# Performance work log

Measured on AMD Instinct MI355X. Metric: run time of the kernel, lower is better.

## Reference

```python
import jax, jax.numpy as jnp
import numpy as np

KS = 5
NF = 64
B, H, W = 2, 160, 160


def _conv1x1(x, w, b):
    # x: (B,Ci,H,W), w: (Co,Ci)
    return jnp.einsum('oi,bihw->bohw', w, x) + b[None, :, None, None]


def _conv2x2(x, w, b, dil):
    # x: (B,1,Hp,Wp), w: (64,1,2,2); VALID conv with dilation dil
    y = jax.lax.conv_general_dilated(x, w, (1, 1), 'VALID',
                                     rhs_dilation=(dil, dil),
                                     dimension_numbers=('NCHW', 'OIHW', 'NCHW'))
    return y + b[None, :, None, None]


def _conv_s(x, w, b):
    # conv1 module, mode 's': gather taps (0,0),(1,1),(1,2),(2,1) of each 3x3 patch,
    # then (1,4) conv == linear combo of 4 shifted images.
    h = x.shape[2] - 2
    wd = x.shape[3] - 2
    x0 = x[:, 0]
    taps = jnp.stack([x0[:, 0:h, 0:wd],
                      x0[:, 1:h + 1, 1:wd + 1],
                      x0[:, 1:h + 1, 2:wd + 2],
                      x0[:, 2:h + 2, 1:wd + 1]], axis=1)  # (B,4,h,wd)
    return jnp.einsum('ok,bkhw->bohw', w.reshape(NF, 4), taps) + b[None, :, None, None]


def _construct(c, dense_ps):
    # relu then dense 1x1-conv chain with channel concat, final 1x1 -> 4 channels
    x = jax.nn.relu(c)
    for (wt, bs) in dense_ps[:-1]:
        feat = jax.nn.relu(_conv1x1(x, wt, bs))
        x = jnp.concatenate([x, feat], axis=1)
    wt, bs = dense_ps[-1]
    return _conv1x1(x, wt, bs)


def _ag(x, sigx, sigy, theta, sigr):
    # x: (B,ks,ks,HW); params: (B,HW). Per-pixel anisotropic bilateral kernel.
    ks = x.shape[1]
    r = jnp.arange(ks, dtype=x.dtype) - ks // 2
    sq = (r[:, None] ** 2 + r[None, :] ** 2)[None, :, :, None]  # (1,ks,ks,1)
    sx = sigx[:, None, None, :]
    sy = sigy[:, None, None, :]
    th = theta[:, None, None, :]
    sr = sigr[:, None, None, :]
    spatial = jnp.exp(-sq / (2.0 * sr ** 2))
    disx = jnp.abs(x[:, ks // 2:ks // 2 + 1] - x)       # center row
    disy = jnp.abs(x[:, :, ks // 2:ks // 2 + 1] - x)    # center col
    a = sx * disx
    bb = sy * disy
    color = jnp.exp(-0.5 * (a ** 2 - 2.0 * th * a * bb + bb ** 2))
    kern = spatial * color
    kern = kern / jnp.sum(kern, axis=(1, 2), keepdims=True)
    return jnp.sum(kern * x, axis=(1, 2))  # (B,HW)


def _forward(x_in, conv1x_w, conv1x_b, conv1c_w, conv1c_b, conv1cs_w, conv1cs_b,
             w2, b2, w3, b3, w4, b4, w5, b5, w6, b6):
    dense_ps = [(w2, b2), (w3, b3), (w4, b4), (w5, b5), (w6, b6)]

    def fk(x, mod):
        if mod == 's':
            c = _conv_s(x, conv1cs_w, conv1cs_b)
        elif mod == 'c':
            c = _conv2x2(x, conv1c_w, conv1c_b, 2)
        else:
            c = _conv2x2(x, conv1x_w, conv1x_b, 1)
        return _construct(c, dense_ps)

    def mode_ens(x, p, mod):
        pad = lambda z: jnp.pad(z, ((0, 0), (0, 0), (0, p), (0, p)), mode='reflect')
        r0 = fk(pad(x), mod)
        r2 = jnp.rot90(fk(pad(jnp.rot90(x, 2, (2, 3))), mod), 2, (2, 3))
        r1 = jnp.rot90(fk(pad(jnp.rot90(x, 1, (2, 3))), mod), 3, (2, 3))
        r3 = jnp.rot90(fk(pad(jnp.rot90(x, 3, (2, 3))), mod), 1, (2, 3))
        return (r0 + r2) / 2.0, (r1 + r3) / 2.0

    e1x, e2x = mode_ens(x_in, 1, 'x')
    e1s, e2s = mode_ens(x_in, 2, 's')
    e1c, e2c = mode_ens(x_in, 2, 'c')
    par = (e1x + e2x + e1s + e2s + e1c + e2c) / 6.0  # (B,4,H,W)

    b, c, h, w = x_in.shape
    sigx = jnp.clip(jax.nn.sigmoid(par[:, 0]).reshape(b, -1) + 1e-6, 0.0, 1.0)
    sigy = jnp.clip(jax.nn.sigmoid(par[:, 1]).reshape(b, -1) + 1e-6, 0.0, 1.0)
    theta = jnp.clip(jnp.tanh(par[:, 2]).reshape(b, -1), -1.0, 1.0)
    sigr = jnp.clip(jnp.tanh(par[:, 3]).reshape(b, -1) + 1e-6, -1.0, 1.0)

    ph = KS // 2
    xt = jnp.pad(x_in, ((0, 0), (0, 0), (ph, ph), (ph, ph)))  # zero pad
    # unfold -> (B, KS, KS, H*W)
    patches = jnp.stack([jnp.stack([xt[:, 0, i:i + h, j:j + w].reshape(b, -1)
                                    for j in range(KS)], axis=1)
                         for i in range(KS)], axis=1)
    outs = _ag(patches, sigx * 20.0, sigy * 20.0, theta, sigr * 10.0 + 10.0).reshape(b, c, h, w)
    return outs, sigx, sigy, theta, sigr


def setup_inputs() -> dict:
    key = jax.random.key(0)
    k = jax.random.split(key, 10)
    def kn(kk, shape, fan_in):
        return jax.random.normal(kk, shape, jnp.float32) * np.float32(np.sqrt(2.0 / fan_in))
    zb = lambda n: jnp.zeros((n,), jnp.float32)
    return {
        'x_in': jax.random.normal(k[0], (B, 1, H, W), jnp.float32),
        'conv1x_w': kn(k[1], (NF, 1, 2, 2), 4), 'conv1x_b': zb(NF),
        'conv1c_w': kn(k[2], (NF, 1, 2, 2), 4), 'conv1c_b': zb(NF),
        'conv1cs_w': kn(k[3], (NF, 1, 1, 4), 4), 'conv1cs_b': zb(NF),
        'w2': kn(k[4], (NF, NF), NF), 'b2': zb(NF),
        'w3': kn(k[5], (NF, 2 * NF), 2 * NF), 'b3': zb(NF),
        'w4': kn(k[6], (NF, 3 * NF), 3 * NF), 'b4': zb(NF),
        'w5': kn(k[7], (NF, 4 * NF), 4 * NF), 'b5': zb(NF),
        'w6': kn(k[8], (4, 5 * NF), 5 * NF), 'b6': zb(4),
    }


def reference(x_in, conv1x_w, conv1x_b, conv1c_w, conv1c_b, conv1cs_w, conv1cs_b,
              w2, b2, w3, b3, w4, b4, w5, b5, w6, b6):
    return _forward(x_in, conv1x_w, conv1x_b, conv1c_w, conv1c_b, conv1cs_w, conv1cs_b,
                    w2, b2, w3, b3, w4, b4, w5, b5, w6, b6)
```

## Files before the change

kernel.cpp:

```cpp
#include <hip/hip_runtime.h>
#include <hip/hip_bf16.h>
#include <math.h>
#include <string.h>


#define NN   160
#define NPIX 25600

typedef __attribute__((ext_vector_type(4))) float float4v;
typedef __attribute__((ext_vector_type(8))) unsigned short ushort8;
typedef __attribute__((ext_vector_type(2))) unsigned int uint2v;
typedef __attribute__((ext_vector_type(4))) unsigned int uint4v;
typedef __attribute__((ext_vector_type(8))) __bf16 bf16x8;

#define PINV(x) asm volatile("" : "+v"(x))

__device__ __forceinline__ int refp(int a) { return (a <= NN - 1) ? a : (2 * (NN - 1) - a); }

__device__ __forceinline__ unsigned int pk2(float lo, float hi) {
    float2 f; f.x = lo; f.y = hi;
    __hip_bfloat162 h = __float22bfloat162_rn(f);
    unsigned int u;
    memcpy(&u, &h, 4);
    return u;
}
__device__ __forceinline__ ushort8 cvt8(const float* __restrict__ p) {
    const float4v f0 = *(const float4v*)p;
    const float4v f1 = *(const float4v*)(p + 4);
    uint4v u;
    u[0] = pk2(f0[0], f0[1]); u[1] = pk2(f0[2], f0[3]);
    u[2] = pk2(f1[0], f1[1]); u[3] = pk2(f1[2], f1[3]);
    return __builtin_bit_cast(ushort8, u);
}

template <int NCH>
__device__ __forceinline__ void dense_layer(const ushort8 (&A)[NCH], float4v biasv,
                                            unsigned short* Xs, int w, int lo16, int lq) {
    const int K = NCH * 32;
#pragma unroll
    for (int pp = 0; pp < 2; ++pp) {
        const int px0 = (pp * 2) * 16 + lo16;
        const int px1 = (pp * 2 + 1) * 16 + lo16;
        float4v acc0 = biasv, acc1 = biasv;
#pragma unroll
        for (int s = 0; s < NCH; ++s) {
            const int c8 = s * 4 + lq;
            const bf16x8 bf0 = __builtin_bit_cast(bf16x8, *(const ushort8*)&Xs[c8 * 512 + px0 * 8]);
            const bf16x8 bf1 = __builtin_bit_cast(bf16x8, *(const ushort8*)&Xs[c8 * 512 + px1 * 8]);
            const bf16x8 af  = __builtin_bit_cast(bf16x8, A[s]);
            acc0 = __builtin_amdgcn_mfma_f32_16x16x32_bf16(af, bf0, acc0, 0, 0, 0);
            acc1 = __builtin_amdgcn_mfma_f32_16x16x32_bf16(af, bf1, acc1, 0, 0, 0);
        }
        const int cb = K + w * 16 + lq * 4;
        uint2v o0, o1;
        o0[0] = pk2(fmaxf(acc0[0], 0.0f), fmaxf(acc0[1], 0.0f));
        o0[1] = pk2(fmaxf(acc0[2], 0.0f), fmaxf(acc0[3], 0.0f));
        o1[0] = pk2(fmaxf(acc1[0], 0.0f), fmaxf(acc1[1], 0.0f));
        o1[1] = pk2(fmaxf(acc1[2], 0.0f), fmaxf(acc1[3], 0.0f));
        *(uint2v*)&Xs[(cb >> 3) * 512 + px0 * 8 + (cb & 7)] = o0;
        *(uint2v*)&Xs[(cb >> 3) * 512 + px1 * 8 + (cb & 7)] = o1;
    }
    __syncthreads();
}

__global__
__attribute__((amdgpu_flat_work_group_size(256, 256)))
__attribute__((amdgpu_waves_per_eu(3, 3)))
void bnet_mlp_kernel(
    const float* __restrict__ x,
    const float* __restrict__ wx, const float* __restrict__ bx,
    const float* __restrict__ wcs, const float* __restrict__ bcs,
    const float* __restrict__ wc, const float* __restrict__ bc,
    const float* __restrict__ w2, const float* __restrict__ b2,
    const float* __restrict__ w3, const float* __restrict__ b3,
    const float* __restrict__ w4, const float* __restrict__ b4,
    const float* __restrict__ w5, const float* __restrict__ b5,
    const float* __restrict__ w6,
    float* __restrict__ par)
{
    __shared__ unsigned short Xs[20480];
    float* red = (float*)Xs;

    const int t = threadIdx.x;
    const int lane = t & 63;
    const int lo16 = lane & 15;
    const int lq = lane >> 4;
    const int w = __builtin_amdgcn_readfirstlane(t >> 6);

    const int arow = w * 16 + lo16;
    ushort8 a2[2], a3[4], a4[6], a5[8], a6[3];
#pragma unroll
    for (int s = 0; s < 2; ++s) { a2[s] = cvt8(&w2[arow * 64 + s * 32 + lq * 8]);  PINV(a2[s]); }
#pragma unroll
    for (int s = 0; s < 4; ++s) { a3[s] = cvt8(&w3[arow * 128 + s * 32 + lq * 8]); PINV(a3[s]); }
#pragma unroll
    for (int s = 0; s < 6; ++s) { a4[s] = cvt8(&w4[arow * 192 + s * 32 + lq * 8]); PINV(a4[s]); }
#pragma unroll
    for (int s = 0; s < 8; ++s) { a5[s] = cvt8(&w5[arow * 256 + s * 32 + lq * 8]); PINV(a5[s]); }
#pragma unroll
    for (int c = 0; c < 3; ++c) {
        const int ch = (3 * w + c) * 32;
        if (ch < 320 && lo16 < 4) {
            a6[c] = cvt8(&w6[lo16 * 320 + ch + lq * 8]);
        } else {
            ushort8 z = {0, 0, 0, 0, 0, 0, 0, 0};
            a6[c] = z;
        }
        PINV(a6[c]);
    }
    const float4v b2v = *(const float4v*)&b2[w * 16 + lq * 4];
    const float4v b3v = *(const float4v*)&b3[w * 16 + lq * 4];
    const float4v b4v = *(const float4v*)&b4[w * 16 + lq * 4];
    const float4v b5v = *(const float4v*)&b5[w * 16 + lq * 4];

    const int bid = blockIdx.x;
    const int nit = 12 + (bid < 384 ? 1 : 0);
    const int g0  = (bid < 384) ? bid * 13 : bid * 12 + 384;

    float4v acc6[4];
    int cur_tb = -1;

    for (int it = 0; it < nit; ++it) {
        const int g = g0 + it;
        const int v = g % 12;
        const int tb = g / 12;
        const int tile = tb >> 1;
        const int b = tb & 1;
        const int mode = v >> 2;
        const int k = v & 3;

        __syncthreads();

        if (tb != cur_tb) {
            if (cur_tb >= 0) {
                const int ftile = cur_tb >> 1;
                const int fb = cur_tb & 1;
                if (lq == 0) {
#pragma unroll
                    for (int pt = 0; pt < 4; ++pt)
                        *(float4v*)&red[(((w * 4) + pt) * 16 + lo16) * 4] = acc6[pt];
                }
                __syncthreads();
                if (w == 0) {
                    float4v sv;
#pragma unroll
                    for (int r = 0; r < 4; ++r)
                        sv[r] = red[(((0 * 4) + lq) * 16 + lo16) * 4 + r]
                              + red[(((1 * 4) + lq) * 16 + lo16) * 4 + r]
                              + red[(((2 * 4) + lq) * 16 + lo16) * 4 + r]
                              + red[(((3 * 4) + lq) * 16 + lo16) * 4 + r];
                    const int pixg = ftile * 64 + lq * 16 + lo16;
#pragma unroll
                    for (int r = 0; r < 4; ++r)
                        atomicAdd(&par[(r * 2 + fb) * NPIX + pixg], sv[r]);
                }
                __syncthreads();
            }
#pragma unroll
            for (int pt = 0; pt < 4; ++pt) { float4v z = {0.f, 0.f, 0.f, 0.f}; acc6[pt] = z; }
            cur_tb = tb;
        }

        const float* xb = x + b * NPIX;
        const float* w1 = (mode == 0) ? wx : (mode == 1) ? wcs : wc;
        const float* b1 = (mode == 0) ? bx : (mode == 1) ? bcs : bc;
        int DY[4], DX[4];
        if (mode == 0)      { DY[0]=0; DY[1]=0; DY[2]=1; DY[3]=1;  DX[0]=0; DX[1]=1; DX[2]=0; DX[3]=1; }
        else if (mode == 1) { DY[0]=0; DY[1]=1; DY[2]=1; DY[3]=2;  DX[0]=0; DX[1]=1; DX[2]=2; DX[3]=1; }
        else                { DY[0]=0; DY[1]=0; DY[2]=2; DY[3]=2;  DX[0]=0; DX[1]=2; DX[2]=0; DX[3]=2; }

        const int pix = tile * 64 + lane;
        const int pi = pix / NN;
        const int pj = pix - pi * NN;

        float s4[4];
#pragma unroll
        for (int tt = 0; tt < 4; ++tt) {
            const int dy = DY[tt], dx = DX[tt];
            int r, c;
            if (k == 0)      { r = refp(pi + dy); c = refp(pj + dx); }
            else if (k == 1) { r = refp(pi + dx); c = (pj >= dy) ? (pj - dy) : (dy - pj); }
            else if (k == 2) { r = (pi >= dy) ? (pi - dy) : (dy - pi);
                               c = (pj >= dx) ? (pj - dx) : (dx - pj); }
            else             { r = (pi >= dx) ? (pi - dx) : (dx - pi); c = refp(pj + dy); }
            s4[tt] = xb[r * NN + c];
        }
        float4v b1v[4];
#pragma unroll
        for (int q = 0; q < 4; ++q) b1v[q] = *(const float4v*)&b1[w * 16 + q * 4];
        float co[16];
#pragma unroll
        for (int oo = 0; oo < 16; ++oo) {
            const int o = w * 16 + oo;
            const float4v wv = *(const float4v*)&w1[o * 4];
            float cacc = b1v[oo >> 2][oo & 3];
#pragma unroll
            for (int tt = 0; tt < 4; ++tt) cacc = fmaf(wv[tt], s4[tt], cacc);
            co[oo] = fmaxf(cacc, 0.0f);
        }
        uint4v pka, pkb;
#pragma unroll
        for (int q = 0; q < 4; ++q) {
            pka[q] = pk2(co[2 * q], co[2 * q + 1]);
            pkb[q] = pk2(co[8 + 2 * q], co[9 + 2 * q]);
        }
        *(uint4v*)&Xs[(w * 2) * 512 + lane * 8]     = pka;
        *(uint4v*)&Xs[(w * 2 + 1) * 512 + lane * 8] = pkb;
        __syncthreads();

        dense_layer<2>(a2, b2v, Xs, w, lo16, lq);
        dense_layer<4>(a3, b3v, Xs, w, lo16, lq);
        dense_layer<6>(a4, b4v, Xs, w, lo16, lq);
        dense_layer<8>(a5, b5v, Xs, w, lo16, lq);

#pragma unroll
        for (int pt = 0; pt < 4; ++pt) {
            const int px = pt * 16 + lo16;
#pragma unroll
            for (int c = 0; c < 3; ++c) {
                int chb = (3 * w + c) * 32;
                chb = (chb < 288) ? chb : 288;
                const int c8 = (chb >> 3) + lq;
                const bf16x8 bf = __builtin_bit_cast(
                    bf16x8, *(const ushort8*)&Xs[c8 * 512 + px * 8]);
                const bf16x8 af = __builtin_bit_cast(bf16x8, a6[c]);
                acc6[pt] = __builtin_amdgcn_mfma_f32_16x16x32_bf16(af, bf, acc6[pt], 0, 0, 0);
            }
        }
    }

    __syncthreads();
    {
        const int ftile = cur_tb >> 1;
        const int fb = cur_tb & 1;
        if (lq == 0) {
#pragma unroll
            for (int pt = 0; pt < 4; ++pt)
                *(float4v*)&red[(((w * 4) + pt) * 16 + lo16) * 4] = acc6[pt];
        }
        __syncthreads();
        if (w == 0) {
            float4v sv;
#pragma unroll
            for (int r = 0; r < 4; ++r)
                sv[r] = red[(((0 * 4) + lq) * 16 + lo16) * 4 + r]
                      + red[(((1 * 4) + lq) * 16 + lo16) * 4 + r]
                      + red[(((2 * 4) + lq) * 16 + lo16) * 4 + r]
                      + red[(((3 * 4) + lq) * 16 + lo16) * 4 + r];
            const int pixg = ftile * 64 + lq * 16 + lo16;
#pragma unroll
            for (int r = 0; r < 4; ++r)
                atomicAdd(&par[(r * 2 + fb) * NPIX + pixg], sv[r]);
        }
    }
}

__global__ __launch_bounds__(64) void bnet_bilateral_kernel(
    const float* __restrict__ x, const float* __restrict__ b6,
    float* __restrict__ out)
{
    const int tid = blockIdx.x * 64 + threadIdx.x;
    const int b = tid / NPIX;
    const int pix = tid - b * NPIX;
    const int pi = pix / NN;
    const int pj = pix - pi * NN;

    float* par = out + 2 * NPIX;
    const float inv12 = 1.0f / 12.0f;
    const float p0 = par[(0 + b) * NPIX + pix] * inv12 + b6[0];
    const float p1 = par[(2 + b) * NPIX + pix] * inv12 + b6[1];
    const float p2 = par[(4 + b) * NPIX + pix] * inv12 + b6[2];
    const float p3 = par[(6 + b) * NPIX + pix] * inv12 + b6[3];

    float sigx = 1.0f / (1.0f + __expf(-p0)) + 1e-6f;
    sigx = fminf(fmaxf(sigx, 0.0f), 1.0f);
    float sigy = 1.0f / (1.0f + __expf(-p1)) + 1e-6f;
    sigy = fminf(fmaxf(sigy, 0.0f), 1.0f);
    float t2 = __expf(2.0f * fminf(fmaxf(p2, -15.0f), 15.0f));
    float th = (t2 - 1.0f) / (t2 + 1.0f);
    th = fminf(fmaxf(th, -1.0f), 1.0f);
    float t3 = __expf(2.0f * fminf(fmaxf(p3, -15.0f), 15.0f));
    float sigr = (t3 - 1.0f) / (t3 + 1.0f) + 1e-6f;
    sigr = fminf(fmaxf(sigr, -1.0f), 1.0f);

    par[(0 + b) * NPIX + pix] = sigx;
    par[(2 + b) * NPIX + pix] = sigy;
    par[(4 + b) * NPIX + pix] = th;
    par[(6 + b) * NPIX + pix] = sigr;

    const float sx = sigx * 20.0f;
    const float sy = sigy * 20.0f;
    const float sr = sigr * 10.0f + 10.0f;

    const float* xb = x + b * NPIX;
    float patch[5][5];
#pragma unroll
    for (int ky = 0; ky < 5; ++ky) {
#pragma unroll
        for (int kx = 0; kx < 5; ++kx) {
            const int r = pi + ky - 2, c = pj + kx - 2;
            patch[ky][kx] = (r >= 0 && r < NN && c >= 0 && c < NN) ? xb[r * NN + c] : 0.0f;
        }
    }

    const float inv2sr2 = 1.0f / (2.0f * sr * sr);
    float num = 0.0f, den = 0.0f;
#pragma unroll
    for (int ky = 0; ky < 5; ++ky) {
#pragma unroll
        for (int kx = 0; kx < 5; ++kx) {
            const float v = patch[ky][kx];
            const float dxv = fabsf(patch[2][kx] - v);
            const float dyv = fabsf(patch[ky][2] - v);
            const float a = sx * dxv;
            const float bb = sy * dyv;
            const float sq = (float)((ky - 2) * (ky - 2) + (kx - 2) * (kx - 2));
            const float kern = __expf(-sq * inv2sr2 - 0.5f * (a * a - 2.0f * th * a * bb + bb * bb));
            den += kern;
            num = fmaf(kern, v, num);
        }
    }
    out[tid] = num / den;
}

extern "C" void kernel_launch(void* const* d_in, const int* in_sizes, int n_in,
                              void* d_out, int out_size, void* d_ws, size_t ws_size,
                              hipStream_t stream) {
    const float* x   = (const float*)d_in[0];
    const float* wx  = (const float*)d_in[1];
    const float* bx  = (const float*)d_in[2];
    const float* wc  = (const float*)d_in[3];
    const float* bc  = (const float*)d_in[4];
    const float* wcs = (const float*)d_in[5];
    const float* bcs = (const float*)d_in[6];
    const float* w2  = (const float*)d_in[7];
    const float* b2  = (const float*)d_in[8];
    const float* w3  = (const float*)d_in[9];
    const float* b3  = (const float*)d_in[10];
    const float* w4  = (const float*)d_in[11];
    const float* b4  = (const float*)d_in[12];
    const float* w5  = (const float*)d_in[13];
    const float* b5  = (const float*)d_in[14];
    const float* w6  = (const float*)d_in[15];
    const float* b6  = (const float*)d_in[16];
    float* out = (float*)d_out;

    (void)hipMemsetAsync(out + 2 * NPIX, 0, 8 * NPIX * sizeof(float), stream);

    hipLaunchKernelGGL(bnet_mlp_kernel, dim3(768), dim3(256), 0, stream,
                       x, wx, bx, wcs, bcs, wc, bc,
                       w2, b2, w3, b3, w4, b4, w5, b5, w6,
                       out + 2 * NPIX);

    hipLaunchKernelGGL(bnet_bilateral_kernel, dim3(800), dim3(64), 0, stream,
                       x, b6, out);
}
```

Measured before the change: 168.0 us.

## Remap MFMA work so each wave covers two output tiles over half the pixels

Each wave of the dense-layer MFMA work now owns two 16-channel output blocks over two 16-pixel groups, instead of one output block over all four groups. Each B-fragment loaded from LDS feeds two MFMAs, which halves LDS reads per MFMA. The cost is doubling the weights held in registers, so occupancy drops to 2 waves per EU and the grid shrinks from 768 to 512 blocks, each doing more iterations. The final 320-channel reduction is split into two halves, so the cross-wave reduction only sums two partials.

```diff
diff --git a/kernel.cpp b/kernel.cpp
--- a/kernel.cpp
+++ b/kernel.cpp
@@ -34,38 +34,42 @@
 }
 
 template <int NCH>
-__device__ __forceinline__ void dense_layer(const ushort8 (&A)[NCH], float4v biasv,
-                                            unsigned short* Xs, int w, int lo16, int lq) {
+__device__ __forceinline__ void dense_layer2(const ushort8 (&A)[2][NCH],
+                                             const float* __restrict__ bL,
+                                             unsigned short* Xs,
+                                             int ow, int pw, int lo16, int lq) {
     const int K = NCH * 32;
-#pragma unroll
-    for (int pp = 0; pp < 2; ++pp) {
-        const int px0 = (pp * 2) * 16 + lo16;
-        const int px1 = (pp * 2 + 1) * 16 + lo16;
-        float4v acc0 = biasv, acc1 = biasv;
+    const float4v bv0 = *(const float4v*)&bL[(2 * ow + 0) * 16 + lq * 4];
+    const float4v bv1 = *(const float4v*)&bL[(2 * ow + 1) * 16 + lq * 4];
+#pragma unroll
+    for (int gi = 0; gi < 2; ++gi) {
+        const int px = (2 * pw + gi) * 16 + lo16;
+        float4v acc0 = bv0, acc1 = bv1;
 #pragma unroll
         for (int s = 0; s < NCH; ++s) {
-            const int c8 = s * 4 + lq;
-            const bf16x8 bf0 = __builtin_bit_cast(bf16x8, *(const ushort8*)&Xs[c8 * 512 + px0 * 8]);
-            const bf16x8 bf1 = __builtin_bit_cast(bf16x8, *(const ushort8*)&Xs[c8 * 512 + px1 * 8]);
-            const bf16x8 af  = __builtin_bit_cast(bf16x8, A[s]);
-            acc0 = __builtin_amdgcn_mfma_f32_16x16x32_bf16(af, bf0, acc0, 0, 0, 0);
-            acc1 = __builtin_amdgcn_mfma_f32_16x16x32_bf16(af, bf1, acc1, 0, 0, 0);
-        }
-        const int cb = K + w * 16 + lq * 4;
+            const bf16x8 bf = __builtin_bit_cast(
+                bf16x8, *(const ushort8*)&Xs[(s * 4 + lq) * 512 + px * 8]);
+            acc0 = __builtin_amdgcn_mfma_f32_16x16x32_bf16(
+                __builtin_bit_cast(bf16x8, A[0][s]), bf, acc0, 0, 0, 0);
+            acc1 = __builtin_amdgcn_mfma_f32_16x16x32_bf16(
+                __builtin_bit_cast(bf16x8, A[1][s]), bf, acc1, 0, 0, 0);
+        }
+        const int cb0 = K + (2 * ow) * 16 + lq * 4;
+        const int cb1 = cb0 + 16;
         uint2v o0, o1;
         o0[0] = pk2(fmaxf(acc0[0], 0.0f), fmaxf(acc0[1], 0.0f));
         o0[1] = pk2(fmaxf(acc0[2], 0.0f), fmaxf(acc0[3], 0.0f));
         o1[0] = pk2(fmaxf(acc1[0], 0.0f), fmaxf(acc1[1], 0.0f));
         o1[1] = pk2(fmaxf(acc1[2], 0.0f), fmaxf(acc1[3], 0.0f));
-        *(uint2v*)&Xs[(cb >> 3) * 512 + px0 * 8 + (cb & 7)] = o0;
-        *(uint2v*)&Xs[(cb >> 3) * 512 + px1 * 8 + (cb & 7)] = o1;
+        *(uint2v*)&Xs[(cb0 >> 3) * 512 + px * 8 + (cb0 & 7)] = o0;
+        *(uint2v*)&Xs[(cb1 >> 3) * 512 + px * 8 + (cb1 & 7)] = o1;
     }
     __syncthreads();
 }
 
 __global__
 __attribute__((amdgpu_flat_work_group_size(256, 256)))
-__attribute__((amdgpu_waves_per_eu(3, 3)))
+__attribute__((amdgpu_waves_per_eu(2, 2)))
 void bnet_mlp_kernel(
     const float* __restrict__ x,
     const float* __restrict__ wx, const float* __restrict__ bx,
@@ -86,21 +90,26 @@
     const int lo16 = lane & 15;
     const int lq = lane >> 4;
     const int w = __builtin_amdgcn_readfirstlane(t >> 6);
-
-    const int arow = w * 16 + lo16;
-    ushort8 a2[2], a3[4], a4[6], a5[8], a6[3];
-#pragma unroll
-    for (int s = 0; s < 2; ++s) { a2[s] = cvt8(&w2[arow * 64 + s * 32 + lq * 8]);  PINV(a2[s]); }
-#pragma unroll
-    for (int s = 0; s < 4; ++s) { a3[s] = cvt8(&w3[arow * 128 + s * 32 + lq * 8]); PINV(a3[s]); }
-#pragma unroll
-    for (int s = 0; s < 6; ++s) { a4[s] = cvt8(&w4[arow * 192 + s * 32 + lq * 8]); PINV(a4[s]); }
-#pragma unroll
-    for (int s = 0; s < 8; ++s) { a5[s] = cvt8(&w5[arow * 256 + s * 32 + lq * 8]); PINV(a5[s]); }
-#pragma unroll
-    for (int c = 0; c < 3; ++c) {
-        const int ch = (3 * w + c) * 32;
-        if (ch < 320 && lo16 < 4) {
+    const int ow = w & 1;
+    const int pw = w >> 1;
+
+    ushort8 a2[2][2], a3[2][4], a4[2][6], a5[2][8], a6[5];
+#pragma unroll
+    for (int ot = 0; ot < 2; ++ot) {
+        const int arow = (2 * ow + ot) * 16 + lo16;
+#pragma unroll
+        for (int s = 0; s < 2; ++s) { a2[ot][s] = cvt8(&w2[arow * 64 + s * 32 + lq * 8]);  PINV(a2[ot][s]); }
+#pragma unroll
+        for (int s = 0; s < 4; ++s) { a3[ot][s] = cvt8(&w3[arow * 128 + s * 32 + lq * 8]); PINV(a3[ot][s]); }
+#pragma unroll
+        for (int s = 0; s < 6; ++s) { a4[ot][s] = cvt8(&w4[arow * 192 + s * 32 + lq * 8]); PINV(a4[ot][s]); }
+#pragma unroll
+        for (int s = 0; s < 8; ++s) { a5[ot][s] = cvt8(&w5[arow * 256 + s * 32 + lq * 8]); PINV(a5[ot][s]); }
+    }
+#pragma unroll
+    for (int c = 0; c < 5; ++c) {
+        const int ch = (ow * 5 + c) * 32;
+        if (lo16 < 4) {
             a6[c] = cvt8(&w6[lo16 * 320 + ch + lq * 8]);
         } else {
             ushort8 z = {0, 0, 0, 0, 0, 0, 0, 0};
@@ -108,16 +117,12 @@
         }
         PINV(a6[c]);
     }
-    const float4v b2v = *(const float4v*)&b2[w * 16 + lq * 4];
-    const float4v b3v = *(const float4v*)&b3[w * 16 + lq * 4];
-    const float4v b4v = *(const float4v*)&b4[w * 16 + lq * 4];
-    const float4v b5v = *(const float4v*)&b5[w * 16 + lq * 4];
 
     const int bid = blockIdx.x;
-    const int nit = 12 + (bid < 384 ? 1 : 0);
-    const int g0  = (bid < 384) ? bid * 13 : bid * 12 + 384;
-
-    float4v acc6[4];
+    const int nit = 18 + (bid < 384 ? 1 : 0);
+    const int g0  = (bid < 384) ? bid * 19 : bid * 18 + 384;
+
+    float4v acc6[2];
     int cur_tb = -1;
 
     for (int it = 0; it < nit; ++it) {
@@ -137,19 +142,16 @@
                 const int fb = cur_tb & 1;
                 if (lq == 0) {
 #pragma unroll
-                    for (int pt = 0; pt < 4; ++pt)
-                        *(float4v*)&red[(((w * 4) + pt) * 16 + lo16) * 4] = acc6[pt];
+                    for (int gi = 0; gi < 2; ++gi)
+                        *(float4v*)&red[(ow * 64 + (2 * pw + gi) * 16 + lo16) * 4] = acc6[gi];
                 }
                 __syncthreads();
                 if (w == 0) {
                     float4v sv;
 #pragma unroll
                     for (int r = 0; r < 4; ++r)
-                        sv[r] = red[(((0 * 4) + lq) * 16 + lo16) * 4 + r]
-                              + red[(((1 * 4) + lq) * 16 + lo16) * 4 + r]
-                              + red[(((2 * 4) + lq) * 16 + lo16) * 4 + r]
-                              + red[(((3 * 4) + lq) * 16 + lo16) * 4 + r];
-                    const int pixg = ftile * 64 + lq * 16 + lo16;
+                        sv[r] = red[(lane) * 4 + r] + red[(64 + lane) * 4 + r];
+                    const int pixg = ftile * 64 + lane;
 #pragma unroll
                     for (int r = 0; r < 4; ++r)
                         atomicAdd(&par[(r * 2 + fb) * NPIX + pixg], sv[r]);
@@ -157,7 +159,7 @@
                 __syncthreads();
             }
 #pragma unroll
-            for (int pt = 0; pt < 4; ++pt) { float4v z = {0.f, 0.f, 0.f, 0.f}; acc6[pt] = z; }
+            for (int gi = 0; gi < 2; ++gi) { float4v z = {0.f, 0.f, 0.f, 0.f}; acc6[gi] = z; }
             cur_tb = tb;
         }
 
@@ -208,23 +210,21 @@
         *(uint4v*)&Xs[(w * 2 + 1) * 512 + lane * 8] = pkb;
         __syncthreads();
 
-        dense_layer<2>(a2, b2v, Xs, w, lo16, lq);
-        dense_layer<4>(a3, b3v, Xs, w, lo16, lq);
-        dense_layer<6>(a4, b4v, Xs, w, lo16, lq);
-        dense_layer<8>(a5, b5v, Xs, w, lo16, lq);
-
-#pragma unroll
-        for (int pt = 0; pt < 4; ++pt) {
-            const int px = pt * 16 + lo16;
-#pragma unroll
-            for (int c = 0; c < 3; ++c) {
-                int chb = (3 * w + c) * 32;
-                chb = (chb < 288) ? chb : 288;
-                const int c8 = (chb >> 3) + lq;
+        dense_layer2<2>(a2, b2, Xs, ow, pw, lo16, lq);
+        dense_layer2<4>(a3, b3, Xs, ow, pw, lo16, lq);
+        dense_layer2<6>(a4, b4, Xs, ow, pw, lo16, lq);
+        dense_layer2<8>(a5, b5, Xs, ow, pw, lo16, lq);
+
+#pragma unroll
+        for (int gi = 0; gi < 2; ++gi) {
+            const int px = (2 * pw + gi) * 16 + lo16;
+#pragma unroll
+            for (int c = 0; c < 5; ++c) {
+                const int c8 = (ow * 5 + c) * 4 + lq;
                 const bf16x8 bf = __builtin_bit_cast(
                     bf16x8, *(const ushort8*)&Xs[c8 * 512 + px * 8]);
-                const bf16x8 af = __builtin_bit_cast(bf16x8, a6[c]);
-                acc6[pt] = __builtin_amdgcn_mfma_f32_16x16x32_bf16(af, bf, acc6[pt], 0, 0, 0);
+                acc6[gi] = __builtin_amdgcn_mfma_f32_16x16x32_bf16(
+                    __builtin_bit_cast(bf16x8, a6[c]), bf, acc6[gi], 0, 0, 0);
             }
         }
     }
@@ -235,19 +235,16 @@
         const int fb = cur_tb & 1;
         if (lq == 0) {
 #pragma unroll
-            for (int pt = 0; pt < 4; ++pt)
-                *(float4v*)&red[(((w * 4) + pt) * 16 + lo16) * 4] = acc6[pt];
+            for (int gi = 0; gi < 2; ++gi)
+                *(float4v*)&red[(ow * 64 + (2 * pw + gi) * 16 + lo16) * 4] = acc6[gi];
         }
         __syncthreads();
         if (w == 0) {
             float4v sv;
 #pragma unroll
             for (int r = 0; r < 4; ++r)
-                sv[r] = red[(((0 * 4) + lq) * 16 + lo16) * 4 + r]
-                      + red[(((1 * 4) + lq) * 16 + lo16) * 4 + r]
-                      + red[(((2 * 4) + lq) * 16 + lo16) * 4 + r]
-                      + red[(((3 * 4) + lq) * 16 + lo16) * 4 + r];
-            const int pixg = ftile * 64 + lq * 16 + lo16;
+                sv[r] = red[(lane) * 4 + r] + red[(64 + lane) * 4 + r];
+            const int pixg = ftile * 64 + lane;
 #pragma unroll
             for (int r = 0; r < 4; ++r)
                 atomicAdd(&par[(r * 2 + fb) * NPIX + pixg], sv[r]);
@@ -347,7 +344,7 @@
 
     (void)hipMemsetAsync(out + 2 * NPIX, 0, 8 * NPIX * sizeof(float), stream);
 
-    hipLaunchKernelGGL(bnet_mlp_kernel, dim3(768), dim3(256), 0, stream,
+    hipLaunchKernelGGL(bnet_mlp_kernel, dim3(512), dim3(256), 0, stream,
                        x, wx, bx, wcs, bcs, wc, bc,
                        w2, b2, w3, b3, w4, b4, w5, b5, w6,
                        out + 2 * NPIX);
```

Result: slower. 187.3 us (+11.5%).

## Pre-convert MLP weights to bf16 in a prep kernel and raise occupancy

Applied to the files above, without the earlier changes.

Adds a small prep kernel that converts the fp32 dense-layer weights to a bf16 MFMA-ready layout in a workspace buffer. The main kernel now loads those weights per layer from global/L2 instead of holding all of them in registers for its whole lifetime. This frees VGPRs, so waves_per_eu goes from 3 to 4 and the grid grows from 768 to 1024 blocks with fewer work items per block. The cost is an extra launch and repeated weight loads inside the loop.

```diff
diff --git a/kernel.cpp b/kernel.cpp
--- a/kernel.cpp
+++ b/kernel.cpp
@@ -6,14 +6,19 @@
 
 #define NN   160
 #define NPIX 25600
+
+#define W2OFF 0
+#define W3OFF 512
+#define W4OFF 1536
+#define W5OFF 3072
+#define W6OFF 5120
+#define WSUNITS 5888
 
 typedef __attribute__((ext_vector_type(4))) float float4v;
 typedef __attribute__((ext_vector_type(8))) unsigned short ushort8;
 typedef __attribute__((ext_vector_type(2))) unsigned int uint2v;
 typedef __attribute__((ext_vector_type(4))) unsigned int uint4v;
 typedef __attribute__((ext_vector_type(8))) __bf16 bf16x8;
-
-#define PINV(x) asm volatile("" : "+v"(x))
 
 __device__ __forceinline__ int refp(int a) { return (a <= NN - 1) ? a : (2 * (NN - 1) - a); }
 
@@ -24,19 +29,55 @@
     memcpy(&u, &h, 4);
     return u;
 }
-__device__ __forceinline__ ushort8 cvt8(const float* __restrict__ p) {
-    const float4v f0 = *(const float4v*)p;
-    const float4v f1 = *(const float4v*)(p + 4);
-    uint4v u;
-    u[0] = pk2(f0[0], f0[1]); u[1] = pk2(f0[2], f0[3]);
-    u[2] = pk2(f1[0], f1[1]); u[3] = pk2(f1[2], f1[3]);
-    return __builtin_bit_cast(ushort8, u);
+
+__global__ __launch_bounds__(256) void bnet_prep_kernel(
+    const float* __restrict__ w2, const float* __restrict__ w3,
+    const float* __restrict__ w4, const float* __restrict__ w5,
+    const float* __restrict__ w6, ushort8* __restrict__ ws)
+{
+    const int u = blockIdx.x * 256 + threadIdx.x;
+    const int lq = u & 3;
+    float src[8];
+    if (u < W6OFF) {
+        const float* wp; int K, rel;
+        if (u < W3OFF)      { wp = w2; K = 64;  rel = u; }
+        else if (u < W4OFF) { wp = w3; K = 128; rel = u - W3OFF; }
+        else if (u < W5OFF) { wp = w4; K = 192; rel = u - W4OFF; }
+        else                { wp = w5; K = 256; rel = u - W5OFF; }
+        const int arow = (rel >> 2) & 63;
+        const int s = rel >> 8;
+        const float* p = &wp[arow * K + s * 32 + lq * 8];
+#pragma unroll
+        for (int e = 0; e < 8; ++e) src[e] = p[e];
+    } else {
+        const int rel = u - W6OFF;
+        const int r = (rel >> 2) & 15;
+        const int c = rel >> 6;
+        if (r < 4 && c < 10) {
+            const float* p = &w6[r * 320 + c * 32 + lq * 8];
+#pragma unroll
+            for (int e = 0; e < 8; ++e) src[e] = p[e];
+        } else {
+#pragma unroll
+            for (int e = 0; e < 8; ++e) src[e] = 0.0f;
+        }
+    }
+    uint4v o;
+    o[0] = pk2(src[0], src[1]); o[1] = pk2(src[2], src[3]);
+    o[2] = pk2(src[4], src[5]); o[3] = pk2(src[6], src[7]);
+    ws[u] = __builtin_bit_cast(ushort8, o);
 }
 
 template <int NCH>
-__device__ __forceinline__ void dense_layer(const ushort8 (&A)[NCH], float4v biasv,
+__device__ __forceinline__ void dense_layer(const ushort8* __restrict__ wsL,
+                                            const float* __restrict__ bL,
                                             unsigned short* Xs, int w, int lo16, int lq) {
     const int K = NCH * 32;
+    const int arow = w * 16 + lo16;
+    ushort8 af[NCH];
+#pragma unroll
+    for (int s = 0; s < NCH; ++s) af[s] = wsL[(s * 64 + arow) * 4 + lq];
+    const float4v biasv = *(const float4v*)&bL[w * 16 + lq * 4];
 #pragma unroll
     for (int pp = 0; pp < 2; ++pp) {
         const int px0 = (pp * 2) * 16 + lo16;
@@ -44,12 +85,11 @@
         float4v acc0 = biasv, acc1 = biasv;
 #pragma unroll
         for (int s = 0; s < NCH; ++s) {
-            const int c8 = s * 4 + lq;
-            const bf16x8 bf0 = __builtin_bit_cast(bf16x8, *(const ushort8*)&Xs[c8 * 512 + px0 * 8]);
-            const bf16x8 bf1 = __builtin_bit_cast(bf16x8, *(const ushort8*)&Xs[c8 * 512 + px1 * 8]);
-            const bf16x8 af  = __builtin_bit_cast(bf16x8, A[s]);
-            acc0 = __builtin_amdgcn_mfma_f32_16x16x32_bf16(af, bf0, acc0, 0, 0, 0);
-            acc1 = __builtin_amdgcn_mfma_f32_16x16x32_bf16(af, bf1, acc1, 0, 0, 0);
+            const bf16x8 bf0 = __builtin_bit_cast(bf16x8, *(const ushort8*)&Xs[(s * 4 + lq) * 512 + px0 * 8]);
+            const bf16x8 bf1 = __builtin_bit_cast(bf16x8, *(const ushort8*)&Xs[(s * 4 + lq) * 512 + px1 * 8]);
+            const bf16x8 afv = __builtin_bit_cast(bf16x8, af[s]);
+            acc0 = __builtin_amdgcn_mfma_f32_16x16x32_bf16(afv, bf0, acc0, 0, 0, 0);
+            acc1 = __builtin_amdgcn_mfma_f32_16x16x32_bf16(afv, bf1, acc1, 0, 0, 0);
         }
         const int cb = K + w * 16 + lq * 4;
         uint2v o0, o1;
@@ -65,17 +105,15 @@
 
 __global__
 __attribute__((amdgpu_flat_work_group_size(256, 256)))
-__attribute__((amdgpu_waves_per_eu(3, 3)))
+__attribute__((amdgpu_waves_per_eu(4, 4)))
 void bnet_mlp_kernel(
     const float* __restrict__ x,
     const float* __restrict__ wx, const float* __restrict__ bx,
     const float* __restrict__ wcs, const float* __restrict__ bcs,
     const float* __restrict__ wc, const float* __restrict__ bc,
-    const float* __restrict__ w2, const float* __restrict__ b2,
-    const float* __restrict__ w3, const float* __restrict__ b3,
-    const float* __restrict__ w4, const float* __restrict__ b4,
-    const float* __restrict__ w5, const float* __restrict__ b5,
-    const float* __restrict__ w6,
+    const float* __restrict__ b2, const float* __restrict__ b3,
+    const float* __restrict__ b4, const float* __restrict__ b5,
+    const ushort8* __restrict__ wsb,
     float* __restrict__ par)
 {
     __shared__ unsigned short Xs[20480];
@@ -87,35 +125,9 @@
     const int lq = lane >> 4;
     const int w = __builtin_amdgcn_readfirstlane(t >> 6);
 
-    const int arow = w * 16 + lo16;
-    ushort8 a2[2], a3[4], a4[6], a5[8], a6[3];
-#pragma unroll
-    for (int s = 0; s < 2; ++s) { a2[s] = cvt8(&w2[arow * 64 + s * 32 + lq * 8]);  PINV(a2[s]); }
-#pragma unroll
-    for (int s = 0; s < 4; ++s) { a3[s] = cvt8(&w3[arow * 128 + s * 32 + lq * 8]); PINV(a3[s]); }
-#pragma unroll
-    for (int s = 0; s < 6; ++s) { a4[s] = cvt8(&w4[arow * 192 + s * 32 + lq * 8]); PINV(a4[s]); }
-#pragma unroll
-    for (int s = 0; s < 8; ++s) { a5[s] = cvt8(&w5[arow * 256 + s * 32 + lq * 8]); PINV(a5[s]); }
-#pragma unroll
-    for (int c = 0; c < 3; ++c) {
-        const int ch = (3 * w + c) * 32;
-        if (ch < 320 && lo16 < 4) {
-            a6[c] = cvt8(&w6[lo16 * 320 + ch + lq * 8]);
-        } else {
-            ushort8 z = {0, 0, 0, 0, 0, 0, 0, 0};
-            a6[c] = z;
-        }
-        PINV(a6[c]);
-    }
-    const float4v b2v = *(const float4v*)&b2[w * 16 + lq * 4];
-    const float4v b3v = *(const float4v*)&b3[w * 16 + lq * 4];
-    const float4v b4v = *(const float4v*)&b4[w * 16 + lq * 4];
-    const float4v b5v = *(const float4v*)&b5[w * 16 + lq * 4];
-
     const int bid = blockIdx.x;
-    const int nit = 12 + (bid < 384 ? 1 : 0);
-    const int g0  = (bid < 384) ? bid * 13 : bid * 12 + 384;
+    const int nit = 9 + (bid < 384 ? 1 : 0);
+    const int g0  = (bid < 384) ? bid * 10 : bid * 9 + 384;
 
     float4v acc6[4];
     int cur_tb = -1;
@@ -208,11 +220,15 @@
         *(uint4v*)&Xs[(w * 2 + 1) * 512 + lane * 8] = pkb;
         __syncthreads();
 
-        dense_layer<2>(a2, b2v, Xs, w, lo16, lq);
-        dense_layer<4>(a3, b3v, Xs, w, lo16, lq);
-        dense_layer<6>(a4, b4v, Xs, w, lo16, lq);
-        dense_layer<8>(a5, b5v, Xs, w, lo16, lq);
-
+        dense_layer<2>(wsb + W2OFF, b2, Xs, w, lo16, lq);
+        dense_layer<4>(wsb + W3OFF, b3, Xs, w, lo16, lq);
+        dense_layer<6>(wsb + W4OFF, b4, Xs, w, lo16, lq);
+        dense_layer<8>(wsb + W5OFF, b5, Xs, w, lo16, lq);
+
+        ushort8 a6[3];
+#pragma unroll
+        for (int c = 0; c < 3; ++c)
+            a6[c] = wsb[W6OFF + ((3 * w + c) * 16 + lo16) * 4 + lq];
 #pragma unroll
         for (int pt = 0; pt < 4; ++pt) {
             const int px = pt * 16 + lo16;
@@ -223,8 +239,8 @@
                 const int c8 = (chb >> 3) + lq;
                 const bf16x8 bf = __builtin_bit_cast(
                     bf16x8, *(const ushort8*)&Xs[c8 * 512 + px * 8]);
-                const bf16x8 af = __builtin_bit_cast(bf16x8, a6[c]);
-                acc6[pt] = __builtin_amdgcn_mfma_f32_16x16x32_bf16(af, bf, acc6[pt], 0, 0, 0);
+                acc6[pt] = __builtin_amdgcn_mfma_f32_16x16x32_bf16(
+                    __builtin_bit_cast(bf16x8, a6[c]), bf, acc6[pt], 0, 0, 0);
             }
         }
     }
@@ -344,12 +360,16 @@
     const float* w6  = (const float*)d_in[15];
     const float* b6  = (const float*)d_in[16];
     float* out = (float*)d_out;
+    ushort8* ws = (ushort8*)d_ws;
 
     (void)hipMemsetAsync(out + 2 * NPIX, 0, 8 * NPIX * sizeof(float), stream);
 
-    hipLaunchKernelGGL(bnet_mlp_kernel, dim3(768), dim3(256), 0, stream,
+    hipLaunchKernelGGL(bnet_prep_kernel, dim3(WSUNITS / 256), dim3(256), 0, stream,
+                       w2, w3, w4, w5, w6, ws);
+
+    hipLaunchKernelGGL(bnet_mlp_kernel, dim3(1024), dim3(256), 0, stream,
                        x, wx, bx, wcs, bcs, wc, bc,
-                       w2, b2, w3, b3, w4, b4, w5, b5, w6,
+                       b2, b3, b4, b5, (const ushort8*)ws,
                        out + 2 * NPIX);
 
     hipLaunchKernelGGL(bnet_bilateral_kernel, dim3(800), dim3(64), 0, stream,
```

Result: slower. 184.3 us (+9.7%).

## Process two work items per iteration with dual LDS buffers to halve barriers

Applied to the files above, without the earlier changes.

Each block now handles two (tile,batch,variant) items per loop iteration, using two LDS activation buffers so every dense layer issues four independent MFMA chains and one barrier covers both items. The grid shrinks from 768 to 512 blocks with 18-19 items each, and the occupancy hint drops from three to two waves per EU to leave room for the extra accumulators. Separate accumulators track two tile-batch groups, which means more frequent flushes with atomics. The intent is to reduce synchronisation and latency stalls per item, at the cost of lower occupancy and doubled LDS use.

```diff
diff --git a/kernel.cpp b/kernel.cpp
--- a/kernel.cpp
+++ b/kernel.cpp
@@ -34,38 +34,126 @@
 }
 
 template <int NCH>
-__device__ __forceinline__ void dense_layer(const ushort8 (&A)[NCH], float4v biasv,
-                                            unsigned short* Xs, int w, int lo16, int lq) {
+__device__ __forceinline__ void dense_dual(const ushort8 (&A)[NCH], float4v biasv,
+                                           unsigned short* X0, unsigned short* X1,
+                                           int w, int lo16, int lq) {
     const int K = NCH * 32;
 #pragma unroll
     for (int pp = 0; pp < 2; ++pp) {
         const int px0 = (pp * 2) * 16 + lo16;
         const int px1 = (pp * 2 + 1) * 16 + lo16;
-        float4v acc0 = biasv, acc1 = biasv;
+        float4v aA0 = biasv, aA1 = biasv, aB0 = biasv, aB1 = biasv;
 #pragma unroll
         for (int s = 0; s < NCH; ++s) {
             const int c8 = s * 4 + lq;
-            const bf16x8 bf0 = __builtin_bit_cast(bf16x8, *(const ushort8*)&Xs[c8 * 512 + px0 * 8]);
-            const bf16x8 bf1 = __builtin_bit_cast(bf16x8, *(const ushort8*)&Xs[c8 * 512 + px1 * 8]);
             const bf16x8 af  = __builtin_bit_cast(bf16x8, A[s]);
-            acc0 = __builtin_amdgcn_mfma_f32_16x16x32_bf16(af, bf0, acc0, 0, 0, 0);
-            acc1 = __builtin_amdgcn_mfma_f32_16x16x32_bf16(af, bf1, acc1, 0, 0, 0);
+            const bf16x8 bA0 = __builtin_bit_cast(bf16x8, *(const ushort8*)&X0[c8 * 512 + px0 * 8]);
+            const bf16x8 bB0 = __builtin_bit_cast(bf16x8, *(const ushort8*)&X1[c8 * 512 + px0 * 8]);
+            const bf16x8 bA1 = __builtin_bit_cast(bf16x8, *(const ushort8*)&X0[c8 * 512 + px1 * 8]);
+            const bf16x8 bB1 = __builtin_bit_cast(bf16x8, *(const ushort8*)&X1[c8 * 512 + px1 * 8]);
+            aA0 = __builtin_amdgcn_mfma_f32_16x16x32_bf16(af, bA0, aA0, 0, 0, 0);
+            aB0 = __builtin_amdgcn_mfma_f32_16x16x32_bf16(af, bB0, aB0, 0, 0, 0);
+            aA1 = __builtin_amdgcn_mfma_f32_16x16x32_bf16(af, bA1, aA1, 0, 0, 0);
+            aB1 = __builtin_amdgcn_mfma_f32_16x16x32_bf16(af, bB1, aB1, 0, 0, 0);
         }
         const int cb = K + w * 16 + lq * 4;
-        uint2v o0, o1;
-        o0[0] = pk2(fmaxf(acc0[0], 0.0f), fmaxf(acc0[1], 0.0f));
-        o0[1] = pk2(fmaxf(acc0[2], 0.0f), fmaxf(acc0[3], 0.0f));
-        o1[0] = pk2(fmaxf(acc1[0], 0.0f), fmaxf(acc1[1], 0.0f));
-        o1[1] = pk2(fmaxf(acc1[2], 0.0f), fmaxf(acc1[3], 0.0f));
-        *(uint2v*)&Xs[(cb >> 3) * 512 + px0 * 8 + (cb & 7)] = o0;
-        *(uint2v*)&Xs[(cb >> 3) * 512 + px1 * 8 + (cb & 7)] = o1;
+        uint2v oA0, oA1, oB0, oB1;
+        oA0[0] = pk2(fmaxf(aA0[0], 0.0f), fmaxf(aA0[1], 0.0f));
+        oA0[1] = pk2(fmaxf(aA0[2], 0.0f), fmaxf(aA0[3], 0.0f));
+        oA1[0] = pk2(fmaxf(aA1[0], 0.0f), fmaxf(aA1[1], 0.0f));
+        oA1[1] = pk2(fmaxf(aA1[2], 0.0f), fmaxf(aA1[3], 0.0f));
+        oB0[0] = pk2(fmaxf(aB0[0], 0.0f), fmaxf(aB0[1], 0.0f));
+        oB0[1] = pk2(fmaxf(aB0[2], 0.0f), fmaxf(aB0[3], 0.0f));
+        oB1[0] = pk2(fmaxf(aB1[0], 0.0f), fmaxf(aB1[1], 0.0f));
+        oB1[1] = pk2(fmaxf(aB1[2], 0.0f), fmaxf(aB1[3], 0.0f));
+        *(uint2v*)&X0[(cb >> 3) * 512 + px0 * 8 + (cb & 7)] = oA0;
+        *(uint2v*)&X0[(cb >> 3) * 512 + px1 * 8 + (cb & 7)] = oA1;
+        *(uint2v*)&X1[(cb >> 3) * 512 + px0 * 8 + (cb & 7)] = oB0;
+        *(uint2v*)&X1[(cb >> 3) * 512 + px1 * 8 + (cb & 7)] = oB1;
+    }
+    __syncthreads();
+}
+
+__device__ __forceinline__ void conv_phase(
+    const float* __restrict__ xb, const float* __restrict__ w1,
+    const float* __restrict__ b1, int tile, int mode, int k,
+    unsigned short* X, int w, int lane, int lo16, int lq)
+{
+    int DY[4], DX[4];
+    if (mode == 0)      { DY[0]=0; DY[1]=0; DY[2]=1; DY[3]=1;  DX[0]=0; DX[1]=1; DX[2]=0; DX[3]=1; }
+    else if (mode == 1) { DY[0]=0; DY[1]=1; DY[2]=1; DY[3]=2;  DX[0]=0; DX[1]=1; DX[2]=2; DX[3]=1; }
+    else                { DY[0]=0; DY[1]=0; DY[2]=2; DY[3]=2;  DX[0]=0; DX[1]=2; DX[2]=0; DX[3]=2; }
+
+    const int pix = tile * 64 + lane;
+    const int pi = pix / NN;
+    const int pj = pix - pi * NN;
+
+    float s4[4];
+#pragma unroll
+    for (int tt = 0; tt < 4; ++tt) {
+        const int dy = DY[tt], dx = DX[tt];
+        int r, c;
+        if (k == 0)      { r = refp(pi + dy); c = refp(pj + dx); }
+        else if (k == 1) { r = refp(pi + dx); c = (pj >= dy) ? (pj - dy) : (dy - pj); }
+        else if (k == 2) { r = (pi >= dy) ? (pi - dy) : (dy - pi);
+                           c = (pj >= dx) ? (pj - dx) : (dx - pj); }
+        else             { r = (pi >= dx) ? (pi - dx) : (dx - pi); c = refp(pj + dy); }
+        s4[tt] = xb[r * NN + c];
+    }
+    float4v b1v[4];
+#pragma unroll
+    for (int q = 0; q < 4; ++q) b1v[q] = *(const float4v*)&b1[w * 16 + q * 4];
+    float co[16];
+#pragma unroll
+    for (int oo = 0; oo < 16; ++oo) {
+        const int o = w * 16 + oo;
+        const float4v wv = *(const float4v*)&w1[o * 4];
+        float cacc = b1v[oo >> 2][oo & 3];
+#pragma unroll
+        for (int tt = 0; tt < 4; ++tt) cacc = fmaf(wv[tt], s4[tt], cacc);
+        co[oo] = fmaxf(cacc, 0.0f);
+    }
+    uint4v pka, pkb;
+#pragma unroll
+    for (int q = 0; q < 4; ++q) {
+        pka[q] = pk2(co[2 * q], co[2 * q + 1]);
+        pkb[q] = pk2(co[8 + 2 * q], co[9 + 2 * q]);
+    }
+    *(uint4v*)&X[(w * 2) * 512 + lane * 8]     = pka;
+    *(uint4v*)&X[(w * 2 + 1) * 512 + lane * 8] = pkb;
+}
+
+__device__ __forceinline__ void flush_tb(const float4v (&acc6)[4], int ftb,
+                                         float* red, float* __restrict__ par,
+                                         int w, int lo16, int lq)
+{
+    const int ftile = ftb >> 1;
+    const int fb = ftb & 1;
+    if (lq == 0) {
+#pragma unroll
+        for (int pt = 0; pt < 4; ++pt)
+            *(float4v*)&red[(((w * 4) + pt) * 16 + lo16) * 4] = acc6[pt];
+    }
+    __syncthreads();
+    if (w == 0) {
+        float4v sv;
+#pragma unroll
+        for (int r = 0; r < 4; ++r)
+            sv[r] = red[(((0 * 4) + lq) * 16 + lo16) * 4 + r]
+                  + red[(((1 * 4) + lq) * 16 + lo16) * 4 + r]
+                  + red[(((2 * 4) + lq) * 16 + lo16) * 4 + r]
+                  + red[(((3 * 4) + lq) * 16 + lo16) * 4 + r];
+        const int pixg = ftile * 64 + lq * 16 + lo16;
+#pragma unroll
+        for (int r = 0; r < 4; ++r)
+            atomicAdd(&par[(r * 2 + fb) * NPIX + pixg], sv[r]);
     }
     __syncthreads();
 }
 
 __global__
 __attribute__((amdgpu_flat_work_group_size(256, 256)))
-__attribute__((amdgpu_waves_per_eu(3, 3)))
+__attribute__((amdgpu_waves_per_eu(2, 2)))
 void bnet_mlp_kernel(
     const float* __restrict__ x,
     const float* __restrict__ wx, const float* __restrict__ bx,
@@ -78,8 +166,8 @@
     const float* __restrict__ w6,
     float* __restrict__ par)
 {
-    __shared__ unsigned short Xs[20480];
-    float* red = (float*)Xs;
+    __shared__ unsigned short Xs[2][20480];
+    float* red = (float*)&Xs[0][0];
 
     const int t = threadIdx.x;
     const int lane = t & 63;
@@ -114,104 +202,50 @@
     const float4v b5v = *(const float4v*)&b5[w * 16 + lq * 4];
 
     const int bid = blockIdx.x;
-    const int nit = 12 + (bid < 384 ? 1 : 0);
-    const int g0  = (bid < 384) ? bid * 13 : bid * 12 + 384;
-
-    float4v acc6[4];
-    int cur_tb = -1;
-
-    for (int it = 0; it < nit; ++it) {
-        const int g = g0 + it;
-        const int v = g % 12;
-        const int tb = g / 12;
-        const int tile = tb >> 1;
-        const int b = tb & 1;
-        const int mode = v >> 2;
-        const int k = v & 3;
+    const int nit = 18 + (bid < 384 ? 1 : 0);
+    const int g0  = (bid < 384) ? bid * 19 : bid * 18 + 384;
+
+    float4v acc6A[4], acc6B[4];
+    int cur_tbA = -1, cur_tbB = -1;
+
+    for (int ii = 0; ii < nit; ii += 2) {
+        const bool dual = (ii + 1 < nit);
+        const int gA = g0 + ii;
+        const int gB = dual ? (gA + 1) : gA;
+
+        const int vA = gA % 12, tbA = gA / 12;
+        const int tileA = tbA >> 1, bA = tbA & 1, modeA = vA >> 2, kA = vA & 3;
+        const int vB = gB % 12, tbB = gB / 12;
+        const int tileB = tbB >> 1, bB = tbB & 1, modeB = vB >> 2, kB = vB & 3;
 
         __syncthreads();
 
-        if (tb != cur_tb) {
-            if (cur_tb >= 0) {
-                const int ftile = cur_tb >> 1;
-                const int fb = cur_tb & 1;
-                if (lq == 0) {
-#pragma unroll
-                    for (int pt = 0; pt < 4; ++pt)
-                        *(float4v*)&red[(((w * 4) + pt) * 16 + lo16) * 4] = acc6[pt];
-                }
-                __syncthreads();
-                if (w == 0) {
-                    float4v sv;
-#pragma unroll
-                    for (int r = 0; r < 4; ++r)
-                        sv[r] = red[(((0 * 4) + lq) * 16 + lo16) * 4 + r]
-                              + red[(((1 * 4) + lq) * 16 + lo16) * 4 + r]
-                              + red[(((2 * 4) + lq) * 16 + lo16) * 4 + r]
-                              + red[(((3 * 4) + lq) * 16 + lo16) * 4 + r];
-                    const int pixg = ftile * 64 + lq * 16 + lo16;
-#pragma unroll
-                    for (int r = 0; r < 4; ++r)
-                        atomicAdd(&par[(r * 2 + fb) * NPIX + pixg], sv[r]);
-                }
-                __syncthreads();
-            }
-#pragma unroll
-            for (int pt = 0; pt < 4; ++pt) { float4v z = {0.f, 0.f, 0.f, 0.f}; acc6[pt] = z; }
-            cur_tb = tb;
-        }
-
-        const float* xb = x + b * NPIX;
-        const float* w1 = (mode == 0) ? wx : (mode == 1) ? wcs : wc;
-        const float* b1 = (mode == 0) ? bx : (mode == 1) ? bcs : bc;
-        int DY[4], DX[4];
-        if (mode == 0)      { DY[0]=0; DY[1]=0; DY[2]=1; DY[3]=1;  DX[0]=0; DX[1]=1; DX[2]=0; DX[3]=1; }
-        else if (mode == 1) { DY[0]=0; DY[1]=1; DY[2]=1; DY[3]=2;  DX[0]=0; DX[1]=1; DX[2]=2; DX[3]=1; }
-        else                { DY[0]=0; DY[1]=0; DY[2]=2; DY[3]=2;  DX[0]=0; DX[1]=2; DX[2]=0; DX[3]=2; }
-
-        const int pix = tile * 64 + lane;
-        const int pi = pix / NN;
-        const int pj = pix - pi * NN;
-
-        float s4[4];
-#pragma unroll
-        for (int tt = 0; tt < 4; ++tt) {
-            const int dy = DY[tt], dx = DX[tt];
-            int r, c;
-            if (k == 0)      { r = refp(pi + dy); c = refp(pj + dx); }
-            else if (k == 1) { r = refp(pi + dx); c = (pj >= dy) ? (pj - dy) : (dy - pj); }
-            else if (k == 2) { r = (pi >= dy) ? (pi - dy) : (dy - pi);
-                               c = (pj >= dx) ? (pj - dx) : (dx - pj); }
-            else             { r = (pi >= dx) ? (pi - dx) : (dx - pi); c = refp(pj + dy); }
-            s4[tt] = xb[r * NN + c];
-        }
-        float4v b1v[4];
-#pragma unroll
-        for (int q = 0; q < 4; ++q) b1v[q] = *(const float4v*)&b1[w * 16 + q * 4];
-        float co[16];
-#pragma unroll
-        for (int oo = 0; oo < 16; ++oo) {
-            const int o = w * 16 + oo;
-            const float4v wv = *(const float4v*)&w1[o * 4];
-            float cacc = b1v[oo >> 2][oo & 3];
-#pragma unroll
-            for (int tt = 0; tt < 4; ++tt) cacc = fmaf(wv[tt], s4[tt], cacc);
-            co[oo] = fmaxf(cacc, 0.0f);
-        }
-        uint4v pka, pkb;
-#pragma unroll
-        for (int q = 0; q < 4; ++q) {
-            pka[q] = pk2(co[2 * q], co[2 * q + 1]);
-            pkb[q] = pk2(co[8 + 2 * q], co[9 + 2 * q]);
-        }
-        *(uint4v*)&Xs[(w * 2) * 512 + lane * 8]     = pka;
-        *(uint4v*)&Xs[(w * 2 + 1) * 512 + lane * 8] = pkb;
+        if (tbA != cur_tbA) {
+            if (cur_tbA >= 0) flush_tb(acc6A, cur_tbA, red, par, w, lo16, lq);
+#pragma unroll
+            for (int pt = 0; pt < 4; ++pt) { float4v z = {0.f, 0.f, 0.f, 0.f}; acc6A[pt] = z; }
+            cur_tbA = tbA;
+        }
+        if (dual && tbB != cur_tbB) {
+            if (cur_tbB >= 0) flush_tb(acc6B, cur_tbB, red, par, w, lo16, lq);
+#pragma unroll
+            for (int pt = 0; pt < 4; ++pt) { float4v z = {0.f, 0.f, 0.f, 0.f}; acc6B[pt] = z; }
+            cur_tbB = tbB;
+        }
+
+        const float* w1A = (modeA == 0) ? wx : (modeA == 1) ? wcs : wc;
+        const float* b1A = (modeA == 0) ? bx : (modeA == 1) ? bcs : bc;
+        const float* w1B = (modeB == 0) ? wx : (modeB == 1) ? wcs : wc;
+        const float* b1B = (modeB == 0) ? bx : (modeB == 1) ? bcs : bc;
+
+        conv_phase(x + bA * NPIX, w1A, b1A, tileA, modeA, kA, &Xs[0][0], w, lane, lo16, lq);
+        conv_phase(x + bB * NPIX, w1B, b1B, tileB, modeB, kB, &Xs[1][0], w, lane, lo16, lq);
         __syncthreads();
 
-        dense_layer<2>(a2, b2v, Xs, w, lo16, lq);
-        dense_layer<4>(a3, b3v, Xs, w, lo16, lq);
-        dense_layer<6>(a4, b4v, Xs, w, lo16, lq);
-        dense_layer<8>(a5, b5v, Xs, w, lo16, lq);
+        dense_dual<2>(a2, b2v, &Xs[0][0], &Xs[1][0], w, lo16, lq);
+        dense_dual<4>(a3, b3v, &Xs[0][0], &Xs[1][0], w, lo16, lq);
+        dense_dual<6>(a4, b4v, &Xs[0][0], &Xs[1][0], w, lo16, lq);
+        dense_dual<8>(a5, b5v, &Xs[0][0], &Xs[1][0], w, lo16, lq);
 
 #pragma unroll
         for (int pt = 0; pt < 4; ++pt) {
@@ -222,37 +256,32 @@
                 chb = (chb < 288) ? chb : 288;
                 const int c8 = (chb >> 3) + lq;
                 const bf16x8 bf = __builtin_bit_cast(
-                    bf16x8, *(const ushort8*)&Xs[c8 * 512 + px * 8]);
-                const bf16x8 af = __builtin_bit_cast(bf16x8, a6[c]);
-                acc6[pt] = __builtin_amdgcn_mfma_f32_16x16x32_bf16(af, bf, acc6[pt], 0, 0, 0);
+                    bf16x8, *(const ushort8*)&Xs[0][c8 * 512 + px * 8]);
+                acc6A[pt] = __builtin_amdgcn_mfma_f32_16x16x32_bf16(
+                    __builtin_bit_cast(bf16x8, a6[c]), bf, acc6A[pt], 0, 0, 0);
             }
         }
+        if (dual) {
+#pragma unroll
+            for (int pt = 0; pt < 4; ++pt) {
+                const int px = pt * 16 + lo16;
+#pragma unroll
+                for (int c = 0; c < 3; ++c) {
+                    int chb = (3 * w + c) * 32;
+                    chb = (chb < 288) ? chb : 288;
+                    const int c8 = (chb >> 3) + lq;
+                    const bf16x8 bf = __builtin_bit_cast(
+                        bf16x8, *(const ushort8*)&Xs[1][c8 * 512 + px * 8]);
+                    acc6B[pt] = __builtin_amdgcn_mfma_f32_16x16x32_bf16(
+                        __builtin_bit_cast(bf16x8, a6[c]), bf, acc6B[pt], 0, 0, 0);
+                }
+            }
+        }
     }
 
     __syncthreads();
-    {
-        const int ftile = cur_tb >> 1;
-        const int fb = cur_tb & 1;
-        if (lq == 0) {
-#pragma unroll
-            for (int pt = 0; pt < 4; ++pt)
-                *(float4v*)&red[(((w * 4) + pt) * 16 + lo16) * 4] = acc6[pt];
-        }
-        __syncthreads();
-        if (w == 0) {
-            float4v sv;
-#pragma unroll
-            for (int r = 0; r < 4; ++r)
-                sv[r] = red[(((0 * 4) + lq) * 16 + lo16) * 4 + r]
-                      + red[(((1 * 4) + lq) * 16 + lo16) * 4 + r]
-                      + red[(((2 * 4) + lq) * 16 + lo16) * 4 + r]
-                      + red[(((3 * 4) + lq) * 16 + lo16) * 4 + r];
-            const int pixg = ftile * 64 + lq * 16 + lo16;
-#pragma unroll
-            for (int r = 0; r < 4; ++r)
-                atomicAdd(&par[(r * 2 + fb) * NPIX + pixg], sv[r]);
-        }
-    }
+    if (cur_tbA >= 0) flush_tb(acc6A, cur_tbA, red, par, w, lo16, lq);
+    if (cur_tbB >= 0) flush_tb(acc6B, cur_tbB, red, par, w, lo16, lq);
 }
 
 __global__ __launch_bounds__(64) void bnet_bilateral_kernel(
@@ -347,7 +376,7 @@
 
     (void)hipMemsetAsync(out + 2 * NPIX, 0, 8 * NPIX * sizeof(float), stream);
 
-    hipLaunchKernelGGL(bnet_mlp_kernel, dim3(768), dim3(256), 0, stream,
+    hipLaunchKernelGGL(bnet_mlp_kernel, dim3(512), dim3(256), 0, stream,
                        x, wx, bx, wcs, bcs, wc, bc,
                        w2, b2, w3, b3, w4, b4, w5, b5, w6,
                        out + 2 * NPIX);
```

After: 181.1 us. +7.8%, slower.
